# Optimization experiments

Hardware: AMD Instinct MI355X
Metric: run time of the kernel (lower is better)

## Reference

```python
import jax, jax.numpy as jnp
import numpy as np

B, N, F, D, H, K, L = 16, 2048, 40, 256, 8, 256, 4
DH = D // H  # 32

def setup_inputs() -> dict:
    key = jax.random.key(0)
    ks = jax.random.split(key, 12)
    rn = lambda k, shp: jax.random.normal(k, shp, dtype=jnp.float32) * 0.02
    return dict(
        x=jax.random.normal(ks[0], (B, N, F), dtype=jnp.float32),
        W_emb=rn(ks[1], (F, D)), b_emb=jnp.zeros((D,), jnp.float32),
        pos=rn(ks[11], (1, N, D)),
        ln0_g=jnp.ones((D,), jnp.float32), ln0_b=jnp.zeros((D,), jnp.float32),
        ln1_g=jnp.ones((L, D), jnp.float32), ln1_b=jnp.zeros((L, D), jnp.float32),
        Wq=rn(ks[2], (L, D, D)), Wk=rn(ks[3], (L, D, D)), Wv=rn(ks[4], (L, D, D)),
        Ek=rn(ks[5], (L, N, K)), Ev=rn(ks[6], (L, N, K)),
        Wo=rn(ks[7], (L, D, D)), bo=jnp.zeros((L, D), jnp.float32),
        ln2_g=jnp.ones((L, D), jnp.float32), ln2_b=jnp.zeros((L, D), jnp.float32),
        W1=rn(ks[8], (L, D, 4 * D)), b1=jnp.zeros((L, 4 * D), jnp.float32),
        W2=rn(ks[9], (L, 4 * D, D)), b2=jnp.zeros((L, D), jnp.float32),
        W_out=rn(ks[10], (D, 1)), b_out=jnp.zeros((1,), jnp.float32))

def _ln(t, g, b, eps=1e-5):
    m = t.mean(-1, keepdims=True)
    v = ((t - m) ** 2).mean(-1, keepdims=True)
    return (t - m) * jax.lax.rsqrt(v + eps) * g + b

def reference(x, W_emb, b_emb, pos, ln0_g, ln0_b, ln1_g, ln1_b, Wq, Wk, Wv,
              Ek, Ev, Wo, bo, ln2_g, ln2_b, W1, b1, W2, b2, W_out, b_out):
    h = x @ W_emb + b_emb + pos          # [B,N,D] embed + learned pos enc
    h = _ln(h, ln0_g, ln0_b)
    scale = DH ** -0.5
    for i in range(L):  # Linformer layer: prenorm attn + prenorm FF, residual
        a = _ln(h, ln1_g[i], ln1_b[i])
        q = (a @ Wq[i]).reshape(B, N, H, DH).transpose(0, 2, 1, 3)            # bhnd
        k = jnp.einsum('bnd,nk->bkd', a @ Wk[i], Ek[i])                        # low-rank proj
        v = jnp.einsum('bnd,nk->bkd', a @ Wv[i], Ev[i])
        k = k.reshape(B, K, H, DH).transpose(0, 2, 1, 3)                       # bhkd
        v = v.reshape(B, K, H, DH).transpose(0, 2, 1, 3)
        attn = jax.nn.softmax(jnp.einsum('bhnd,bhkd->bhnk', q, k) * scale, axis=-1)
        o = jnp.einsum('bhnk,bhkd->bhnd', attn, v).transpose(0, 2, 1, 3).reshape(B, N, D)
        h = h + o @ Wo[i] + bo[i]
        a = _ln(h, ln2_g[i], ln2_b[i])
        h = h + jax.nn.gelu(a @ W1[i] + b1[i], approximate=False) @ W2[i] + b2[i]
    return h @ W_out + b_out             # [B,N,1]
```

## Files before the change

kernel.cpp:

```cpp
#include <hip/hip_runtime.h>
#include <hip/hip_bf16.h>


typedef short bf16x8 __attribute__((ext_vector_type(8)));
typedef float f32x4 __attribute__((ext_vector_type(4)));
typedef unsigned int u32x4 __attribute__((ext_vector_type(4)));

#define GLOBAL_AS __attribute__((address_space(1)))
#define LDS_AS __attribute__((address_space(3)))

static __device__ __forceinline__ float gelu_f(float v) {
    const float u2 = v * (0.7978845608028654f + 0.03567740814183427f * v * v);
    const float t = 1.0f - 2.0f / (__expf(2.0f * u2) + 1.0f);
    return 0.5f * v * (1.0f + t);
}
static __device__ __forceinline__ ushort f2bf(float x) {
    __hip_bfloat16 h = __float2bfloat16(x);
    return __builtin_bit_cast(ushort, h);
}

__global__ __launch_bounds__(256)
void embed_ln3(const float* __restrict__ x, const float* __restrict__ Wemb,
               const float* __restrict__ bemb, const float* __restrict__ pos,
               const float* __restrict__ g0, const float* __restrict__ b0,
               float* __restrict__ H)
{
    __shared__ float xs[32][40];
    const int t = threadIdx.x, w = t >> 6, l = t & 63;
    const long row0 = (long)blockIdx.x * 32;
    for (int idx = t; idx < 32 * 40; idx += 256)
        ((float*)xs)[idx] = x[row0 * 40 + idx];
    __syncthreads();

    const int r0 = w * 8;
    const int nbase = (int)((row0 + r0) & 2047);
    const float4 be = *(const float4*)&bemb[l * 4];
    float4 acc[8];
    #pragma unroll 8
    for (int j = 0; j < 8; ++j) {
        const float4 pv = *(const float4*)&pos[(long)(nbase + j) * 256 + l * 4];
        acc[j].x = be.x + pv.x; acc[j].y = be.y + pv.y;
        acc[j].z = be.z + pv.z; acc[j].w = be.w + pv.w;
    }
    for (int f = 0; f < 40; ++f) {
        const float4 wv = *(const float4*)&Wemb[f * 256 + l * 4];
        #pragma unroll 8
        for (int j = 0; j < 8; ++j) {
            const float xf = xs[r0 + j][f];
            acc[j].x += xf * wv.x; acc[j].y += xf * wv.y;
            acc[j].z += xf * wv.z; acc[j].w += xf * wv.w;
        }
    }
    const float4 gv = *(const float4*)&g0[l * 4];
    const float4 bv = *(const float4*)&b0[l * 4];
    #pragma unroll 8
    for (int j = 0; j < 8; ++j) {
        float s = acc[j].x + acc[j].y + acc[j].z + acc[j].w;
        #pragma unroll
        for (int m = 32; m >= 1; m >>= 1) s += __shfl_xor(s, m);
        const float mean = s * (1.0f / 256.0f);
        const float dx = acc[j].x - mean, dy = acc[j].y - mean;
        const float dz = acc[j].z - mean, dw = acc[j].w - mean;
        float q = dx * dx + dy * dy + dz * dz + dw * dw;
        #pragma unroll
        for (int m = 32; m >= 1; m >>= 1) q += __shfl_xor(q, m);
        const float inv = rsqrtf(q * (1.0f / 256.0f) + 1e-5f);
        float4 y;
        y.x = dx * inv * gv.x + bv.x;
        y.y = dy * inv * gv.y + bv.y;
        y.z = dz * inv * gv.z + bv.z;
        y.w = dw * inv * gv.w + bv.w;
        *(float4*)&H[(row0 + r0 + j) * 256 + l * 4] = y;
    }
}

__global__ __launch_bounds__(256)
void ln_kernel(const float* __restrict__ X, const float* __restrict__ g,
               const float* __restrict__ b, ushort* __restrict__ Y)
{
    const int row = blockIdx.x * 4 + (threadIdx.x >> 6);
    const int lane = threadIdx.x & 63;
    const long base = (long)row * 256 + lane * 4;
    float4 xv = *(const float4*)&X[base];
    float s = xv.x + xv.y + xv.z + xv.w;
    #pragma unroll
    for (int m = 32; m >= 1; m >>= 1) s += __shfl_xor(s, m);
    const float mean = s * (1.0f / 256.0f);
    const float dx = xv.x - mean, dy = xv.y - mean, dz = xv.z - mean, dw = xv.w - mean;
    float q = dx * dx + dy * dy + dz * dz + dw * dw;
    #pragma unroll
    for (int m = 32; m >= 1; m >>= 1) q += __shfl_xor(q, m);
    const float inv = rsqrtf(q * (1.0f / 256.0f) + 1e-5f);
    const float4 gv = *(const float4*)&g[lane * 4];
    const float4 bv = *(const float4*)&b[lane * 4];
    ushort4 y;
    y.x = f2bf(dx * inv * gv.x + bv.x);
    y.y = f2bf(dy * inv * gv.y + bv.y);
    y.z = f2bf(dz * inv * gv.z + bv.z);
    y.w = f2bf(dw * inv * gv.w + bv.w);
    *(ushort4*)&Y[base] = y;
}

__global__ __launch_bounds__(256)
void transpose_cast(const float* __restrict__ in, ushort* __restrict__ out,
                    int R, int C, long sIn, long sOut)
{
    __shared__ float tile[32][33];
    in += (long)blockIdx.z * sIn; out += (long)blockIdx.z * sOut;
    const int c0 = blockIdx.x * 32, r0 = blockIdx.y * 32;
    const int tx = threadIdx.x & 31, ty = threadIdx.x >> 5;
    #pragma unroll
    for (int j = 0; j < 4; ++j)
        tile[ty + j * 8][tx] = in[(long)(r0 + ty + j * 8) * C + c0 + tx];
    __syncthreads();
    #pragma unroll
    for (int j = 0; j < 4; ++j)
        out[(long)(c0 + ty + j * 8) * R + r0 + tx] = f2bf(tile[tx][ty + j * 8]);
}

__global__ __launch_bounds__(256)
void transpose_act(const ushort* __restrict__ in, ushort* __restrict__ out)
{
    __shared__ ushort tile[32][33];
    const int c0 = blockIdx.x * 32, r0 = blockIdx.y * 32;
    const int tx = threadIdx.x & 31, ty = threadIdx.x >> 5;
    #pragma unroll
    for (int j = 0; j < 4; ++j)
        tile[ty + j * 8][tx] = in[(long)(r0 + ty + j * 8) * 256 + c0 + tx];
    __syncthreads();
    const int b = r0 >> 11, nn = r0 & 2047;
    #pragma unroll
    for (int j = 0; j < 4; ++j)
        out[((long)(b * 256 + c0 + ty + j * 8)) * 2048 + nn + tx] = tile[tx][ty + j * 8];
}

template<int OBF16, int ACT, int HASB, int ACCF>
__global__ __launch_bounds__(256)
void gemm64(const ushort* __restrict__ A, const ushort* __restrict__ BT,
            const float* __restrict__ bias, void* __restrict__ Cout,
            int Kd, int lda, int ldb, int ldc,
            long sA, long sBT, long sC)
{
    __shared__ ushort Als[2][64 * 32];
    __shared__ ushort Bls[2][64 * 32];
    const int bz = blockIdx.z;
    const ushort* Ab = A + (long)bz * sA;
    const ushort* Bb = BT + (long)bz * sBT;
    const int m0 = blockIdx.x * 64, n0 = blockIdx.y * 64;
    const int t = threadIdx.x, l = t & 63, w = t >> 6;
    const int wr = w >> 1, wc = w & 1;
    const int fr = l & 15, fq = l >> 4;

    f32x4 acc[2][2];
    #pragma unroll
    for (int m = 0; m < 2; ++m)
        #pragma unroll
        for (int n = 0; n < 2; ++n) acc[m][n] = f32x4{0.f, 0.f, 0.f, 0.f};

    const int lrow_off = (l >> 2);
    const int lk_off = (((l & 3) ^ ((l >> 3) & 3)) * 8);
    const int c0c = 2 * w, c1c = 2 * w + 1;
    const int h0 = c0c >> 2, rb0 = (c0c & 3) * 16;
    const int h1 = c1c >> 2, rb1 = (c1c & 3) * 16;
    const ushort* Ag0 = Ab + (long)(m0 + rb0 + lrow_off) * lda + h0 * 32 + lk_off;
    const ushort* Ag1 = Ab + (long)(m0 + rb1 + lrow_off) * lda + h1 * 32 + lk_off;
    const ushort* Bg0 = Bb + (long)(n0 + rb0 + lrow_off) * ldb + h0 * 32 + lk_off;
    const ushort* Bg1 = Bb + (long)(n0 + rb1 + lrow_off) * ldb + h1 * 32 + lk_off;
    const int ad0 = rb0 * 32, ad1 = rb1 * 32;

    const int ks = ((fq ^ ((fr >> 1) & 3)) * 8);

    for (int kk = 0; kk < Kd; kk += 64) {
        __builtin_amdgcn_global_load_lds((const GLOBAL_AS void*)(Ag0 + kk),
                                         (LDS_AS void*)&Als[h0][ad0], 16, 0, 0);
        __builtin_amdgcn_global_load_lds((const GLOBAL_AS void*)(Ag1 + kk),
                                         (LDS_AS void*)&Als[h1][ad1], 16, 0, 0);
        __builtin_amdgcn_global_load_lds((const GLOBAL_AS void*)(Bg0 + kk),
                                         (LDS_AS void*)&Bls[h0][ad0], 16, 0, 0);
        __builtin_amdgcn_global_load_lds((const GLOBAL_AS void*)(Bg1 + kk),
                                         (LDS_AS void*)&Bls[h1][ad1], 16, 0, 0);
        __syncthreads();
        bf16x8 af[2][2], bfv[2][2];
        #pragma unroll
        for (int hh = 0; hh < 2; ++hh) {
            #pragma unroll
            for (int m = 0; m < 2; ++m)
                af[m][hh] = *(const bf16x8*)&Als[hh][(wr * 32 + m * 16 + fr) * 32 + ks];
            #pragma unroll
            for (int n = 0; n < 2; ++n)
                bfv[n][hh] = *(const bf16x8*)&Bls[hh][(wc * 32 + n * 16 + fr) * 32 + ks];
        }
        #pragma unroll
        for (int hh = 0; hh < 2; ++hh)
            #pragma unroll
            for (int m = 0; m < 2; ++m)
                #pragma unroll
                for (int n = 0; n < 2; ++n)
                    acc[m][n] = __builtin_amdgcn_mfma_f32_16x16x32_bf16(
                        af[m][hh], bfv[n][hh], acc[m][n], 0, 0, 0);
        __syncthreads();
    }

    float bsv[2];
    #pragma unroll
    for (int n = 0; n < 2; ++n) bsv[n] = HASB ? bias[n0 + wc * 32 + n * 16 + fr] : 0.f;
    #pragma unroll
    for (int m = 0; m < 2; ++m) {
        #pragma unroll
        for (int r = 0; r < 4; ++r) {
            const int grow = m0 + wr * 32 + m * 16 + fq * 4 + r;
            const long rowoff = (long)grow * ldc + n0 + wc * 32 + fr;
            #pragma unroll
            for (int n = 0; n < 2; ++n) {
                float v = acc[m][n][r] + bsv[n];
                if (ACT) v = gelu_f(v);
                const long off = rowoff + n * 16;
                if (OBF16) {
                    ((ushort*)Cout)[(long)bz * sC + off] = f2bf(v);
                } else {
                    float* Cp = (float*)Cout + (long)bz * sC;
                    if (ACCF) v += Cp[off];
                    Cp[off] = v;
                }
            }
        }
    }
}

__global__ __launch_bounds__(256)
void attn_mfma2(const ushort* __restrict__ Q, const ushort* __restrict__ Kp,
                const ushort* __restrict__ VpT, ushort* __restrict__ O)
{
    __shared__ ushort Kls[256 * 40];
    __shared__ ushort Vls[32 * 264];
    const int qt = blockIdx.x, h = blockIdx.y, b = blockIdx.z;
    const int n0 = qt * 64;
    const int t = threadIdx.x, w = t >> 6, l = t & 63;
    const int fr = l & 15, fq = l >> 4;

    #pragma unroll
    for (int it = 0; it < 4; ++it) {
        const int r = (t >> 2) + it * 64, c = (t & 3) * 8;
        *(float4*)&Kls[r * 40 + c] =
            *(const float4*)&Kp[((long)(b * 256 + r)) * 256 + h * 32 + c];
    }
    {
        const int r = t >> 3, c0 = (t & 7) * 32;
        const ushort* src = VpT + ((long)(b * 256 + h * 32 + r)) * 256 + c0;
        #pragma unroll
        for (int j = 0; j < 4; ++j)
            *(float4*)&Vls[r * 264 + c0 + j * 8] = *(const float4*)(src + j * 8);
    }
    const bf16x8 bq = *(const bf16x8*)
        &Q[((long)(b * 2048 + n0 + w * 16 + fr)) * 256 + h * 32 + fq * 8];
    __syncthreads();

    f32x4 s[16];
    #pragma unroll
    for (int n = 0; n < 16; ++n) {
        const bf16x8 ak = *(const bf16x8*)&Kls[(n * 16 + fr) * 40 + fq * 8];
        s[n] = __builtin_amdgcn_mfma_f32_16x16x32_bf16(ak, bq, f32x4{0.f,0.f,0.f,0.f}, 0, 0, 0);
    }
    const float scale = 0.17677669529663687f;
    float mx = -1e30f;
    #pragma unroll
    for (int n = 0; n < 16; ++n)
        #pragma unroll
        for (int r = 0; r < 4; ++r) { s[n][r] *= scale; mx = fmaxf(mx, s[n][r]); }
    mx = fmaxf(mx, __shfl_xor(mx, 16));
    mx = fmaxf(mx, __shfl_xor(mx, 32));
    float sm = 0.f;
    unsigned int p[16][2];
    #pragma unroll
    for (int n = 0; n < 16; ++n) {
        float e0 = __expf(s[n][0] - mx), e1 = __expf(s[n][1] - mx);
        float e2 = __expf(s[n][2] - mx), e3 = __expf(s[n][3] - mx);
        sm += (e0 + e1) + (e2 + e3);
        p[n][0] = ((unsigned int)f2bf(e1) << 16) | f2bf(e0);
        p[n][1] = ((unsigned int)f2bf(e3) << 16) | f2bf(e2);
    }
    sm += __shfl_xor(sm, 16);
    sm += __shfl_xor(sm, 32);

    const int fqa = fq & 1, fqb = fq >> 1;
    f32x4 o[2] = {f32x4{0.f,0.f,0.f,0.f}, f32x4{0.f,0.f,0.f,0.f}};
    #pragma unroll
    for (int kk = 0; kk < 8; ++kk) {
        u32x4 bw;
        #pragma unroll
        for (int wd = 0; wd < 4; ++wd) {
            const int srcl = fr + ((2 * fqa + (wd >> 1)) << 4);
            const unsigned int v0 = __shfl((int)p[2 * kk][wd & 1], srcl);
            const unsigned int v1 = __shfl((int)p[2 * kk + 1][wd & 1], srcl);
            bw[wd] = fqb ? v1 : v0;
        }
        const bf16x8 breg = __builtin_bit_cast(bf16x8, bw);
        #pragma unroll
        for (int nd = 0; nd < 2; ++nd) {
            const bf16x8 av = *(const bf16x8*)&Vls[(nd * 16 + fr) * 264 + kk * 32 + fq * 8];
            o[nd] = __builtin_amdgcn_mfma_f32_16x16x32_bf16(av, breg, o[nd], 0, 0, 0);
        }
    }
    const float inv = 1.0f / sm;
    const long rowbase = ((long)(b * 2048 + n0 + w * 16 + fr)) * 256 + h * 32;
    #pragma unroll
    for (int nd = 0; nd < 2; ++nd) {
        ushort4 y;
        y.x = f2bf(o[nd][0] * inv); y.y = f2bf(o[nd][1] * inv);
        y.z = f2bf(o[nd][2] * inv); y.w = f2bf(o[nd][3] * inv);
        *(ushort4*)&O[rowbase + nd * 16 + fq * 4] = y;
    }
}

__global__ __launch_bounds__(256)
void out_kernel(const float* __restrict__ H, const float* __restrict__ Wout,
                const float* __restrict__ bout, float* __restrict__ out)
{
    const int row = blockIdx.x * 4 + (threadIdx.x >> 6);
    const int lane = threadIdx.x & 63;
    float4 hv = *(const float4*)&H[(long)row * 256 + lane * 4];
    float4 wv = *(const float4*)&Wout[lane * 4];
    float s = hv.x * wv.x + hv.y * wv.y + hv.z * wv.z + hv.w * wv.w;
    #pragma unroll
    for (int m = 32; m >= 1; m >>= 1) s += __shfl_xor(s, m);
    if (lane == 0) out[row] = s + bout[0];
}

extern "C" void kernel_launch(void* const* d_in, const int* in_sizes, int n_in,
                              void* d_out, int out_size, void* d_ws, size_t ws_size,
                              hipStream_t stream)
{
    const float* x    = (const float*)d_in[0];
    const float* Wemb = (const float*)d_in[1];
    const float* bemb = (const float*)d_in[2];
    const float* pos  = (const float*)d_in[3];
    const float* ln0g = (const float*)d_in[4];
    const float* ln0b = (const float*)d_in[5];
    const float* ln1g = (const float*)d_in[6];
    const float* ln1b = (const float*)d_in[7];
    const float* Wq   = (const float*)d_in[8];
    const float* Wk   = (const float*)d_in[9];
    const float* Wv   = (const float*)d_in[10];
    const float* Ek   = (const float*)d_in[11];
    const float* Ev   = (const float*)d_in[12];
    const float* Wo   = (const float*)d_in[13];
    const float* bo   = (const float*)d_in[14];
    const float* ln2g = (const float*)d_in[15];
    const float* ln2b = (const float*)d_in[16];
    const float* W1   = (const float*)d_in[17];
    const float* b1   = (const float*)d_in[18];
    const float* W2   = (const float*)d_in[19];
    const float* b2   = (const float*)d_in[20];
    const float* Wout = (const float*)d_in[21];
    const float* bout = (const float*)d_in[22];

    char* ws = (char*)d_ws;
    float*  h    = (float*)(ws + 0);
    ushort* abf  = (ushort*)(ws + 33554432L);
    ushort* aT   = (ushort*)(ws + 50331648L);
    ushort* kp   = (ushort*)(ws + 67108864L);
    ushort* vpT  = (ushort*)(ws + 69206016L);
    ushort* apkv = (ushort*)(ws + 71303168L);
    ushort* qbf  = (ushort*)(ws + 100663296L);
    ushort* hid  = (ushort*)(ws + 50331648L);
    ushort* WT   = (ushort*)(ws + 117440512L);
    ushort* WqT  = WT;
    ushort* WkT  = WT + 262144;
    ushort* WvT  = WT + 524288;
    ushort* WoT  = WT + 786432;
    ushort* W1T  = WT + 1048576;
    ushort* W2T  = WT + 2097152;
    ushort* EkvT = WT + 3145728;
    float* outp = (float*)d_out;

    transpose_cast<<<dim3(8, 8, 4), 256, 0, stream>>>(Wq, WqT, 256, 256, 65536, 65536);
    transpose_cast<<<dim3(8, 8, 4), 256, 0, stream>>>(Wk, WkT, 256, 256, 65536, 65536);
    transpose_cast<<<dim3(8, 8, 4), 256, 0, stream>>>(Wv, WvT, 256, 256, 65536, 65536);
    transpose_cast<<<dim3(8, 8, 4), 256, 0, stream>>>(Wo, WoT, 256, 256, 65536, 65536);
    transpose_cast<<<dim3(32, 8, 4), 256, 0, stream>>>(W1, W1T, 256, 1024, 262144, 262144);
    transpose_cast<<<dim3(8, 32, 4), 256, 0, stream>>>(W2, W2T, 1024, 256, 262144, 262144);
    transpose_cast<<<dim3(8, 64, 4), 256, 0, stream>>>(Ek, EkvT, 2048, 256, 524288, 1048576);
    transpose_cast<<<dim3(8, 64, 4), 256, 0, stream>>>(Ev, EkvT + 524288, 2048, 256, 524288, 1048576);

    embed_ln3<<<1024, 256, 0, stream>>>(x, Wemb, bemb, pos, ln0g, ln0b, h);
    ln_kernel<<<8192, 256, 0, stream>>>(h, ln1g, ln1b, abf);
    transpose_act<<<dim3(8, 1024), 256, 0, stream>>>(abf, aT);

    for (int i = 0; i < 4; ++i) {
        const ushort* WqT_i = WqT + i * 65536;
        const ushort* WkT_i = WkT + i * 65536;
        const ushort* WvT_i = WvT + i * 65536;
        const ushort* WoT_i = WoT + i * 65536;
        const ushort* W1T_i = W1T + i * 262144;
        const ushort* W2T_i = W2T + i * 262144;
        const ushort* EkvT_i = EkvT + (long)i * 1048576;

        gemm64<1,0,0,0><<<dim3(512, 4, 1), 256, 0, stream>>>(abf, WqT_i, nullptr, qbf,
            256, 256, 256, 256, 0, 0, 0);
        gemm64<1,0,0,0><<<dim3(8, 4, 16), 256, 0, stream>>>(EkvT_i, aT, nullptr, apkv,
            2048, 2048, 2048, 256, 0, 524288, 131072);
        gemm64<1,0,0,0><<<dim3(4, 4, 16), 256, 0, stream>>>(apkv, WkT_i, nullptr, kp,
            256, 256, 256, 256, 131072, 0, 65536);
        gemm64<1,0,0,0><<<dim3(4, 4, 16), 256, 0, stream>>>(WvT_i, apkv + 65536, nullptr, vpT,
            256, 256, 256, 256, 0, 131072, 65536);
        attn_mfma2<<<dim3(32, 8, 16), 256, 0, stream>>>(qbf, kp, vpT, abf);
        gemm64<0,0,1,1><<<dim3(512, 4, 1), 256, 0, stream>>>(abf, WoT_i, bo + i * 256, h,
            256, 256, 256, 256, 0, 0, 0);
        ln_kernel<<<8192, 256, 0, stream>>>(h, ln2g + i * 256, ln2b + i * 256, abf);
        gemm64<1,1,1,0><<<dim3(512, 16, 1), 256, 0, stream>>>(abf, W1T_i,
            b1 + (long)i * 1024, hid, 256, 256, 256, 1024, 0, 0, 0);
        gemm64<0,0,1,1><<<dim3(512, 4, 1), 256, 0, stream>>>(hid, W2T_i, b2 + i * 256, h,
            1024, 1024, 1024, 256, 0, 0, 0);
        if (i < 3) {
            ln_kernel<<<8192, 256, 0, stream>>>(h, ln1g + (i + 1) * 256,
                ln1b + (i + 1) * 256, abf);
            transpose_act<<<dim3(8, 1024), 256, 0, stream>>>(abf, aT);
        }
    }
    out_kernel<<<8192, 256, 0, stream>>>(h, Wout, bout, outp);
}
```

Baseline: 887.1 us.

## Store residual stream in bf16 and fuse LayerNorm with activation transpose

Switches the residual hidden state from fp32 to bf16 throughout: embedding, residual-accumulating GEMM epilogues, LayerNorms and the output projection all read and write bf16. This halves memory traffic on the largest repeatedly accessed tensor. It also fuses the pre-attention LayerNorm with the transpose needed by the low-rank projection, removing a kernel and a round trip of the normalized activations. The cost is accuracy: residual sums are rounded to bf16 at every layer.

```diff
diff --git a/kernel.cpp b/kernel.cpp
--- a/kernel.cpp
+++ b/kernel.cpp
@@ -18,12 +18,16 @@
     __hip_bfloat16 h = __float2bfloat16(x);
     return __builtin_bit_cast(ushort, h);
 }
+static __device__ __forceinline__ float bf2f(ushort u) {
+    unsigned int x = ((unsigned int)u) << 16;
+    return __builtin_bit_cast(float, x);
+}
 
 __global__ __launch_bounds__(256)
 void embed_ln3(const float* __restrict__ x, const float* __restrict__ Wemb,
                const float* __restrict__ bemb, const float* __restrict__ pos,
                const float* __restrict__ g0, const float* __restrict__ b0,
-               float* __restrict__ H)
+               ushort* __restrict__ H)
 {
     __shared__ float xs[32][40];
     const int t = threadIdx.x, w = t >> 6, l = t & 63;
@@ -65,23 +69,25 @@
         #pragma unroll
         for (int m = 32; m >= 1; m >>= 1) q += __shfl_xor(q, m);
         const float inv = rsqrtf(q * (1.0f / 256.0f) + 1e-5f);
-        float4 y;
-        y.x = dx * inv * gv.x + bv.x;
-        y.y = dy * inv * gv.y + bv.y;
-        y.z = dz * inv * gv.z + bv.z;
-        y.w = dw * inv * gv.w + bv.w;
-        *(float4*)&H[(row0 + r0 + j) * 256 + l * 4] = y;
-    }
-}
-
-__global__ __launch_bounds__(256)
-void ln_kernel(const float* __restrict__ X, const float* __restrict__ g,
-               const float* __restrict__ b, ushort* __restrict__ Y)
+        ushort4 y;
+        y.x = f2bf(dx * inv * gv.x + bv.x);
+        y.y = f2bf(dy * inv * gv.y + bv.y);
+        y.z = f2bf(dz * inv * gv.z + bv.z);
+        y.w = f2bf(dw * inv * gv.w + bv.w);
+        *(ushort4*)&H[(row0 + r0 + j) * 256 + l * 4] = y;
+    }
+}
+
+__global__ __launch_bounds__(256)
+void ln_bf(const ushort* __restrict__ X, const float* __restrict__ g,
+           const float* __restrict__ b, ushort* __restrict__ Y)
 {
     const int row = blockIdx.x * 4 + (threadIdx.x >> 6);
     const int lane = threadIdx.x & 63;
     const long base = (long)row * 256 + lane * 4;
-    float4 xv = *(const float4*)&X[base];
+    const ushort4 xu = *(const ushort4*)&X[base];
+    float4 xv;
+    xv.x = bf2f(xu.x); xv.y = bf2f(xu.y); xv.z = bf2f(xu.z); xv.w = bf2f(xu.w);
     float s = xv.x + xv.y + xv.z + xv.w;
     #pragma unroll
     for (int m = 32; m >= 1; m >>= 1) s += __shfl_xor(s, m);
@@ -102,6 +108,50 @@
 }
 
 __global__ __launch_bounds__(256)
+void ln_tr(const ushort* __restrict__ X, const float* __restrict__ g,
+           const float* __restrict__ b, ushort* __restrict__ Y,
+           ushort* __restrict__ aT)
+{
+    __shared__ ushort tile[32 * 258];
+    const int t = threadIdx.x, w = t >> 6, l = t & 63;
+    const long row0 = (long)blockIdx.x * 32;
+    const float4 gv = *(const float4*)&g[l * 4];
+    const float4 bv = *(const float4*)&b[l * 4];
+    #pragma unroll 8
+    for (int j = 0; j < 8; ++j) {
+        const int r = w * 8 + j;
+        const long base = (row0 + r) * 256 + l * 4;
+        const ushort4 xu = *(const ushort4*)&X[base];
+        float4 xv;
+        xv.x = bf2f(xu.x); xv.y = bf2f(xu.y); xv.z = bf2f(xu.z); xv.w = bf2f(xu.w);
+        float s = xv.x + xv.y + xv.z + xv.w;
+        #pragma unroll
+        for (int m = 32; m >= 1; m >>= 1) s += __shfl_xor(s, m);
+        const float mean = s * (1.0f / 256.0f);
+        const float dx = xv.x - mean, dy = xv.y - mean, dz = xv.z - mean, dw = xv.w - mean;
+        float q = dx * dx + dy * dy + dz * dz + dw * dw;
+        #pragma unroll
+        for (int m = 32; m >= 1; m >>= 1) q += __shfl_xor(q, m);
+        const float inv = rsqrtf(q * (1.0f / 256.0f) + 1e-5f);
+        ushort4 y;
+        y.x = f2bf(dx * inv * gv.x + bv.x);
+        y.y = f2bf(dy * inv * gv.y + bv.y);
+        y.z = f2bf(dz * inv * gv.z + bv.z);
+        y.w = f2bf(dw * inv * gv.w + bv.w);
+        *(ushort4*)&Y[base] = y;
+        *(ushort4*)&tile[r * 258 + l * 4] = y;
+    }
+    __syncthreads();
+    const int tx = t & 31, ty = t >> 5;
+    const int b_ = (int)(row0 >> 11), nn = (int)(row0 & 2047);
+    #pragma unroll 8
+    for (int jj = 0; jj < 32; ++jj) {
+        const int c = ty * 32 + jj;
+        aT[((long)(b_ * 256 + c)) * 2048 + nn + tx] = tile[tx * 258 + c];
+    }
+}
+
+__global__ __launch_bounds__(256)
 void transpose_cast(const float* __restrict__ in, ushort* __restrict__ out,
                     int R, int C, long sIn, long sOut)
 {
@@ -118,26 +168,10 @@
         out[(long)(c0 + ty + j * 8) * R + r0 + tx] = f2bf(tile[tx][ty + j * 8]);
 }
 
-__global__ __launch_bounds__(256)
-void transpose_act(const ushort* __restrict__ in, ushort* __restrict__ out)
-{
-    __shared__ ushort tile[32][33];
-    const int c0 = blockIdx.x * 32, r0 = blockIdx.y * 32;
-    const int tx = threadIdx.x & 31, ty = threadIdx.x >> 5;
-    #pragma unroll
-    for (int j = 0; j < 4; ++j)
-        tile[ty + j * 8][tx] = in[(long)(r0 + ty + j * 8) * 256 + c0 + tx];
-    __syncthreads();
-    const int b = r0 >> 11, nn = r0 & 2047;
-    #pragma unroll
-    for (int j = 0; j < 4; ++j)
-        out[((long)(b * 256 + c0 + ty + j * 8)) * 2048 + nn + tx] = tile[tx][ty + j * 8];
-}
-
-template<int OBF16, int ACT, int HASB, int ACCF>
+template<int ACT, int HASB, int ACCF>
 __global__ __launch_bounds__(256)
 void gemm64(const ushort* __restrict__ A, const ushort* __restrict__ BT,
-            const float* __restrict__ bias, void* __restrict__ Cout,
+            const float* __restrict__ bias, ushort* __restrict__ Cout,
             int Kd, int lda, int ldb, int ldc,
             long sA, long sBT, long sC)
 {
@@ -167,7 +201,6 @@
     const ushort* Bg0 = Bb + (long)(n0 + rb0 + lrow_off) * ldb + h0 * 32 + lk_off;
     const ushort* Bg1 = Bb + (long)(n0 + rb1 + lrow_off) * ldb + h1 * 32 + lk_off;
     const int ad0 = rb0 * 32, ad1 = rb1 * 32;
-
     const int ks = ((fq ^ ((fr >> 1) & 3)) * 8);
 
     for (int kk = 0; kk < Kd; kk += 64) {
@@ -204,6 +237,7 @@
     float bsv[2];
     #pragma unroll
     for (int n = 0; n < 2; ++n) bsv[n] = HASB ? bias[n0 + wc * 32 + n * 16 + fr] : 0.f;
+    ushort* Cp = Cout + (long)bz * sC;
     #pragma unroll
     for (int m = 0; m < 2; ++m) {
         #pragma unroll
@@ -215,13 +249,8 @@
                 float v = acc[m][n][r] + bsv[n];
                 if (ACT) v = gelu_f(v);
                 const long off = rowoff + n * 16;
-                if (OBF16) {
-                    ((ushort*)Cout)[(long)bz * sC + off] = f2bf(v);
-                } else {
-                    float* Cp = (float*)Cout + (long)bz * sC;
-                    if (ACCF) v += Cp[off];
-                    Cp[off] = v;
-                }
+                if (ACCF) v += bf2f(Cp[off]);
+                Cp[off] = f2bf(v);
             }
         }
     }
@@ -313,14 +342,15 @@
 }
 
 __global__ __launch_bounds__(256)
-void out_kernel(const float* __restrict__ H, const float* __restrict__ Wout,
+void out_kernel(const ushort* __restrict__ H, const float* __restrict__ Wout,
                 const float* __restrict__ bout, float* __restrict__ out)
 {
     const int row = blockIdx.x * 4 + (threadIdx.x >> 6);
     const int lane = threadIdx.x & 63;
-    float4 hv = *(const float4*)&H[(long)row * 256 + lane * 4];
+    const ushort4 hu = *(const ushort4*)&H[(long)row * 256 + lane * 4];
     float4 wv = *(const float4*)&Wout[lane * 4];
-    float s = hv.x * wv.x + hv.y * wv.y + hv.z * wv.z + hv.w * wv.w;
+    float s = bf2f(hu.x) * wv.x + bf2f(hu.y) * wv.y +
+              bf2f(hu.z) * wv.z + bf2f(hu.w) * wv.w;
     #pragma unroll
     for (int m = 32; m >= 1; m >>= 1) s += __shfl_xor(s, m);
     if (lane == 0) out[row] = s + bout[0];
@@ -355,7 +385,7 @@
     const float* bout = (const float*)d_in[22];
 
     char* ws = (char*)d_ws;
-    float*  h    = (float*)(ws + 0);
+    ushort* h    = (ushort*)(ws + 0);
     ushort* abf  = (ushort*)(ws + 33554432L);
     ushort* aT   = (ushort*)(ws + 50331648L);
     ushort* kp   = (ushort*)(ws + 67108864L);
@@ -383,8 +413,7 @@
     transpose_cast<<<dim3(8, 64, 4), 256, 0, stream>>>(Ev, EkvT + 524288, 2048, 256, 524288, 1048576);
 
     embed_ln3<<<1024, 256, 0, stream>>>(x, Wemb, bemb, pos, ln0g, ln0b, h);
-    ln_kernel<<<8192, 256, 0, stream>>>(h, ln1g, ln1b, abf);
-    transpose_act<<<dim3(8, 1024), 256, 0, stream>>>(abf, aT);
+    ln_tr<<<1024, 256, 0, stream>>>(h, ln1g, ln1b, abf, aT);
 
     for (int i = 0; i < 4; ++i) {
         const ushort* WqT_i = WqT + i * 65536;
@@ -395,27 +424,25 @@
         const ushort* W2T_i = W2T + i * 262144;
         const ushort* EkvT_i = EkvT + (long)i * 1048576;
 
-        gemm64<1,0,0,0><<<dim3(512, 4, 1), 256, 0, stream>>>(abf, WqT_i, nullptr, qbf,
+        gemm64<0,0,0><<<dim3(512, 4, 1), 256, 0, stream>>>(abf, WqT_i, nullptr, qbf,
             256, 256, 256, 256, 0, 0, 0);
-        gemm64<1,0,0,0><<<dim3(8, 4, 16), 256, 0, stream>>>(EkvT_i, aT, nullptr, apkv,
+        gemm64<0,0,0><<<dim3(8, 4, 16), 256, 0, stream>>>(EkvT_i, aT, nullptr, apkv,
             2048, 2048, 2048, 256, 0, 524288, 131072);
-        gemm64<1,0,0,0><<<dim3(4, 4, 16), 256, 0, stream>>>(apkv, WkT_i, nullptr, kp,
+        gemm64<0,0,0><<<dim3(4, 4, 16), 256, 0, stream>>>(apkv, WkT_i, nullptr, kp,
             256, 256, 256, 256, 131072, 0, 65536);
-        gemm64<1,0,0,0><<<dim3(4, 4, 16), 256, 0, stream>>>(WvT_i, apkv + 65536, nullptr, vpT,
+        gemm64<0,0,0><<<dim3(4, 4, 16), 256, 0, stream>>>(WvT_i, apkv + 65536, nullptr, vpT,
             256, 256, 256, 256, 0, 131072, 65536);
         attn_mfma2<<<dim3(32, 8, 16), 256, 0, stream>>>(qbf, kp, vpT, abf);
-        gemm64<0,0,1,1><<<dim3(512, 4, 1), 256, 0, stream>>>(abf, WoT_i, bo + i * 256, h,
+        gemm64<0,1,1><<<dim3(512, 4, 1), 256, 0, stream>>>(abf, WoT_i, bo + i * 256, h,
             256, 256, 256, 256, 0, 0, 0);
-        ln_kernel<<<8192, 256, 0, stream>>>(h, ln2g + i * 256, ln2b + i * 256, abf);
-        gemm64<1,1,1,0><<<dim3(512, 16, 1), 256, 0, stream>>>(abf, W1T_i,
+        ln_bf<<<8192, 256, 0, stream>>>(h, ln2g + i * 256, ln2b + i * 256, abf);
+        gemm64<1,1,0><<<dim3(512, 16, 1), 256, 0, stream>>>(abf, W1T_i,
             b1 + (long)i * 1024, hid, 256, 256, 256, 1024, 0, 0, 0);
-        gemm64<0,0,1,1><<<dim3(512, 4, 1), 256, 0, stream>>>(hid, W2T_i, b2 + i * 256, h,
+        gemm64<0,1,1><<<dim3(512, 4, 1), 256, 0, stream>>>(hid, W2T_i, b2 + i * 256, h,
             1024, 1024, 1024, 256, 0, 0, 0);
-        if (i < 3) {
-            ln_kernel<<<8192, 256, 0, stream>>>(h, ln1g + (i + 1) * 256,
-                ln1b + (i + 1) * 256, abf);
-            transpose_act<<<dim3(8, 1024), 256, 0, stream>>>(abf, aT);
-        }
+        if (i < 3)
+            ln_tr<<<1024, 256, 0, stream>>>(h, ln1g + (i + 1) * 256,
+                ln1b + (i + 1) * 256, abf, aT);
     }
     out_kernel<<<8192, 256, 0, stream>>>(h, Wout, bout, outp);
 }
```

New measurement: 812.0 us. -8.5%, faster.
